# Kernel tuning notes

Hardware: AMD Instinct MI355X
Metric: run time of the kernel (lower is better)

## Reference

```python
import jax, jax.numpy as jnp
import numpy as np

_COLORS = np.array([
    [255, 255, 255], [219, 178, 187], [210, 144, 98], [230, 79, 56], [207, 62, 108],
    [130, 44, 28], [91, 31, 58], [209, 215, 63], [194, 202, 119], [224, 148, 36],
    [105, 147, 29], [131, 104, 50], [115, 233, 72], [189, 211, 189], [109, 215, 133],
    [72, 131, 77], [69, 81, 65], [77, 212, 193], [101, 159, 190], [120, 142, 215],
    [121, 102, 215], [111, 42, 240], [75, 42, 185], [57, 41, 119], [42, 46, 71],
    [216, 129, 199], [214, 67, 205], [147, 107, 128], [136, 48, 133], [0, 0, 0],
], dtype=np.float32) / 255.0  # [30, 3]

KH, KW = 5, 5
STRIDE = 1
EPS = 1e-8
NORM = 25.0 * 768.0


def _extract_patches(x, kh, kw, s):
    # x: [B, C, H, W] -> patches [B, C, h, w, kh, kw] (valid padding, stride s)
    B, C, H, W = x.shape
    h = (H - kh) // s + 1
    w = (W - kw) // s + 1
    cols = [x[:, :, i:i + s * h:s, j:j + s * w:s] for i in range(kh) for j in range(kw)]
    return jnp.stack(cols, axis=-1).reshape(B, C, h, w, kh, kw)


def setup_inputs() -> dict:
    key = jax.random.key(0)
    input_tensor = jax.random.uniform(key, (8, 3, 224, 224), dtype=jnp.float32)
    # learned parameter: 30 RGB prototype colors tiled over the kernel window
    weight = jnp.asarray(np.tile(_COLORS[:, :, None, None], (1, 1, KH, KW)))  # [30,3,5,5]
    return {"input_tensor": input_tensor, "weight": weight}


def reference(input_tensor, weight):
    kh, kw = weight.shape[2], weight.shape[3]
    p = _extract_patches(input_tensor, kh, kw, STRIDE)  # [B,3,h,w,kh,kw]
    # windows: [B,1,h,w,kh,kw]; weights: [1,30,1,1,kh,kw] -> broadcast [B,30,h,w,kh,kw]
    R1 = p[:, 0][:, None] * 255.0
    G1 = p[:, 1][:, None] * 255.0
    B1 = p[:, 2][:, None] * 255.0
    w255 = weight * 255.0
    R2 = w255[:, 0][None, :, None, None]
    G2 = w255[:, 1][None, :, None, None]
    B2 = w255[:, 2][None, :, None, None]
    rmean = (R1 + R2) * 0.5
    dR = R1 - R2
    dG = G1 - G2
    dB = B1 - B2
    d = jnp.sqrt((2.0 + rmean / 256.0) * dR * dR
                 + 4.0 * dG * dG
                 + (2.0 + (255.0 - rmean) / 256.0) * dB * dB
                 + EPS)
    return d.sum(axis=(-2, -1)) / NORM  # [B, 30, h, w]
```

## Files before the change

### kernel.cpp

```cpp
#include <hip/hip_runtime.h>
#include <hip/hip_fp16.h>
#include <math.h>

#define HDIM 224
#define WDIM 224
#define HW (HDIM * WDIM)
#define OH 220
#define OW 220
#define NCOL 30
#define TY 8
#define DROWS 12
#define NC4 56
#define NCELL (DROWS * NC4)
#define WSTR 116
#define NTILE 28
#define SCALE (16.0f / (25.0f * 768.0f))

__device__ __forceinline__ float4 ld4(const float* p) {
    return *reinterpret_cast<const float4*>(p);
}
__device__ __forceinline__ uint32_t h2u(__half2 h) { return __builtin_bit_cast(uint32_t, h); }
__device__ __forceinline__ __half2 u2h(uint32_t u) { return __builtin_bit_cast(__half2, u); }

__global__ __launch_bounds__(256, 8) void rgb_conv2d_kernel(
    const float* __restrict__ in,
    const float* __restrict__ wt,
    float* __restrict__ out)
{
    __shared__ uint32_t Dd[DROWS * WSTR];

    const int tid = threadIdx.x;
    const int by  = blockIdx.x;
    const int bc  = blockIdx.y;
    const int y0  = (by < NTILE - 1) ? by * TY : (OH - TY);
    const int b   = bc / NCOL;
    const int c   = bc - b * NCOL;

    const float* inb = in + (size_t)b * 3 * HW;
    const float R2f = wt[c * 75 +  0] * 255.0f;
    const float G2f = wt[c * 75 + 25] * 255.0f;
    const float B2f = wt[c * 75 + 50] * 255.0f;

    const __half2 hS    = __float2half2_rn(15.9375f);
    const __half2 hSG   = __float2half2_rn(31.875f);
    const __half2 hC512 = __float2half2_rn(255.0f / 512.0f);
    const __half2 hKR   = __float2half2_rn(fmaf(R2f, 1.0f / 512.0f, 2.0f));
    const __half2 hCC   = __float2half2_rn(4.0f + 255.0f / 256.0f);
    const __half2 hmR   = __float2half2_rn(-R2f * (1.0f / 16.0f));
    const __half2 hmG   = __float2half2_rn(-G2f * (1.0f / 8.0f));
    const __half2 hmB   = __float2half2_rn(-B2f * (1.0f / 16.0f));

    auto dist2 = [&](__half2 r, __half2 g, __half2 bb) -> __half2 {
        __half2 dR = __hfma2(r, hS, hmR);
        __half2 cR = __hfma2(r, hC512, hKR);
        __half2 cB = __hsub2(hCC, cR);
        __half2 dG = __hfma2(g, hSG, hmG);
        __half2 dB = __hfma2(bb, hS, hmB);
        __half2 t  = __hmul2(__hmul2(cR, dR), dR);
        t = __hfma2(dG, dG, t);
        t = __hfma2(__hmul2(cB, dB), dB, t);
        return h2sqrt(t);
    };

    #pragma unroll
    for (int p = 0; p < 3; ++p) {
        int idx = tid + p * 256;
        if (p < 2 || idx < NCELL) {
            int row  = idx / NC4;
            int col4 = idx - row * NC4;
            const float* src = inb + (y0 + row) * WDIM + 4 * col4;
            float4 Pr = ld4(src);
            float4 Pg = ld4(src + HW);
            float4 Pb = ld4(src + 2 * HW);
            __half2 rA = __floats2half2_rn(Pr.x, Pr.y), rB = __floats2half2_rn(Pr.z, Pr.w);
            __half2 gA = __floats2half2_rn(Pg.x, Pg.y), gB = __floats2half2_rn(Pg.z, Pg.w);
            __half2 bA = __floats2half2_rn(Pb.x, Pb.y), bB = __floats2half2_rn(Pb.z, Pb.w);
            __half2 dA = dist2(rA, gA, bA);
            __half2 dB = dist2(rB, gB, bB);
            *reinterpret_cast<uint2*>(&Dd[row * WSTR + 2 * col4]) =
                make_uint2(h2u(dA), h2u(dB));
        }
    }
    __syncthreads();

    if (tid < 220) {
        const int tx = tid % 55;
        const int g2 = tid / 55;
        const uint32_t* dp = &Dd[(2 * g2) * WSTR + 2 * tx];

        __half2 HA[6], HB[6];
        #pragma unroll
        for (int r = 0; r < 6; ++r) {
            uint2 v0 = *reinterpret_cast<const uint2*>(dp + r * WSTR);
            uint2 v1 = *reinterpret_cast<const uint2*>(dp + r * WSTR + 2);
            uint32_t a = v0.x, bw = v0.y, cw = v1.x, e = v1.y;
            __half2 t1 = u2h(__builtin_amdgcn_alignbit(bw, a, 16));
            __half2 t2 = u2h(__builtin_amdgcn_alignbit(cw, bw, 16));
            __half2 t3 = u2h(__builtin_amdgcn_alignbit(e, cw, 16));
            __half2 s  = __hadd2(__hadd2(u2h(bw), t2), u2h(cw));
            HA[r] = __hadd2(s, __hadd2(u2h(a), t1));
            HB[r] = __hadd2(s, __hadd2(t3, u2h(e)));
        }

        __half2 VA0 = __hadd2(__hadd2(__hadd2(HA[0], HA[1]), __hadd2(HA[2], HA[3])), HA[4]);
        __half2 VB0 = __hadd2(__hadd2(__hadd2(HB[0], HB[1]), __hadd2(HB[2], HB[3])), HB[4]);
        __half2 VA1 = __hadd2(__hsub2(VA0, HA[0]), HA[5]);
        __half2 VB1 = __hadd2(__hsub2(VB0, HB[0]), HB[5]);

        float* ob = out + ((size_t)bc * OH + (y0 + 2 * g2)) * OW + 4 * tx;
        *reinterpret_cast<float4*>(ob) =
            make_float4(__low2float(VA0) * SCALE, __high2float(VA0) * SCALE,
                        __low2float(VB0) * SCALE, __high2float(VB0) * SCALE);
        *reinterpret_cast<float4*>(ob + OW) =
            make_float4(__low2float(VA1) * SCALE, __high2float(VA1) * SCALE,
                        __low2float(VB1) * SCALE, __high2float(VB1) * SCALE);
    }
}

extern "C" void kernel_launch(void* const* d_in, const int* in_sizes, int n_in,
                              void* d_out, int out_size, void* d_ws, size_t ws_size,
                              hipStream_t stream) {
    const float* in = (const float*)d_in[0];
    const float* wt = (const float*)d_in[1];
    float* out = (float*)d_out;

    const int B = in_sizes[0] / (3 * HW);
    dim3 grid(NTILE, B * NCOL);
    rgb_conv2d_kernel<<<grid, dim3(256), 0, stream>>>(in, wt, out);
}
```

Before: 21.65 us.

## Process 55-row panels per block with persistent loop and nontemporal stores

Each block now covers a 55-row panel in five 11-row iterations instead of a single 8-row tile. That cuts the halo recompute overhead from 12/8 to 15/11 rows and lowers the block count. The grid is 1D with batch as the fastest index, so blocks that share a color are spread over different images. Outputs go out through nontemporal stores. The cost is an extra barrier per iteration, less parallelism, and uneven 3- or 2-row output work per thread group.

```diff
diff --git a/kernel.cpp b/kernel.cpp
--- a/kernel.cpp
+++ b/kernel.cpp
@@ -1,6 +1,5 @@
 #include <hip/hip_runtime.h>
 #include <hip/hip_fp16.h>
-#include <math.h>
 
 #define HDIM 224
 #define WDIM 224
@@ -8,13 +7,16 @@
 #define OH 220
 #define OW 220
 #define NCOL 30
-#define TY 8
-#define DROWS 12
+#define TY 11
+#define DROWS 15
 #define NC4 56
 #define NCELL (DROWS * NC4)
 #define WSTR 116
-#define NTILE 28
+#define NIT 5
+#define PANEL 55
 #define SCALE (16.0f / (25.0f * 768.0f))
+
+typedef float f4 __attribute__((ext_vector_type(4)));
 
 __device__ __forceinline__ float4 ld4(const float* p) {
     return *reinterpret_cast<const float4*>(p);
@@ -22,21 +24,31 @@
 __device__ __forceinline__ uint32_t h2u(__half2 h) { return __builtin_bit_cast(uint32_t, h); }
 __device__ __forceinline__ __half2 u2h(uint32_t u) { return __builtin_bit_cast(__half2, u); }
 
-__global__ __launch_bounds__(256, 8) void rgb_conv2d_kernel(
+__device__ __forceinline__ void st_nt(float* p, __half2 a, __half2 b) {
+    f4 v = { __low2float(a) * SCALE, __high2float(a) * SCALE,
+             __low2float(b) * SCALE, __high2float(b) * SCALE };
+    __builtin_nontemporal_store(v, reinterpret_cast<f4*>(p));
+}
+
+__global__ __launch_bounds__(256) void rgb_conv2d_kernel(
     const float* __restrict__ in,
     const float* __restrict__ wt,
-    float* __restrict__ out)
+    float* __restrict__ out,
+    int B)
 {
     __shared__ uint32_t Dd[DROWS * WSTR];
 
     const int tid = threadIdx.x;
-    const int by  = blockIdx.x;
-    const int bc  = blockIdx.y;
-    const int y0  = (by < NTILE - 1) ? by * TY : (OH - TY);
-    const int b   = bc / NCOL;
-    const int c   = bc - b * NCOL;
+    const int L   = blockIdx.x;
+    const int b   = L % B;
+    const int j   = L / B;
+    const int c   = j >> 2;
+    const int by  = j & 3;
+    const int y0  = by * PANEL;
 
     const float* inb = in + (size_t)b * 3 * HW;
+    const int bc = b * NCOL + c;
+
     const float R2f = wt[c * 75 +  0] * 255.0f;
     const float G2f = wt[c * 75 + 25] * 255.0f;
     const float B2f = wt[c * 75 + 50] * 255.0f;
@@ -62,58 +74,67 @@
         return h2sqrt(t);
     };
 
-    #pragma unroll
-    for (int p = 0; p < 3; ++p) {
-        int idx = tid + p * 256;
-        if (p < 2 || idx < NCELL) {
-            int row  = idx / NC4;
-            int col4 = idx - row * NC4;
-            const float* src = inb + (y0 + row) * WDIM + 4 * col4;
-            float4 Pr = ld4(src);
-            float4 Pg = ld4(src + HW);
-            float4 Pb = ld4(src + 2 * HW);
-            __half2 rA = __floats2half2_rn(Pr.x, Pr.y), rB = __floats2half2_rn(Pr.z, Pr.w);
-            __half2 gA = __floats2half2_rn(Pg.x, Pg.y), gB = __floats2half2_rn(Pg.z, Pg.w);
-            __half2 bA = __floats2half2_rn(Pb.x, Pb.y), bB = __floats2half2_rn(Pb.z, Pb.w);
-            __half2 dA = dist2(rA, gA, bA);
-            __half2 dB = dist2(rB, gB, bB);
-            *reinterpret_cast<uint2*>(&Dd[row * WSTR + 2 * col4]) =
-                make_uint2(h2u(dA), h2u(dB));
+    const int tx = tid % 55;
+    const int g  = tid / 55;
+    const int rg = 3 * g;
+    const int nr = (g < 3) ? 3 : 2;
+
+    for (int it = 0; it < NIT; ++it) {
+        const int yb = y0 + it * TY;
+
+        #pragma unroll
+        for (int p = 0; p < 4; ++p) {
+            int idx = tid + p * 256;
+            if (p < 3 || idx < NCELL) {
+                int row  = idx / NC4;
+                int col4 = idx - row * NC4;
+                const float* src = inb + (yb + row) * WDIM + 4 * col4;
+                float4 Pr = ld4(src);
+                float4 Pg = ld4(src + HW);
+                float4 Pb = ld4(src + 2 * HW);
+                __half2 rA = __floats2half2_rn(Pr.x, Pr.y), rB = __floats2half2_rn(Pr.z, Pr.w);
+                __half2 gA = __floats2half2_rn(Pg.x, Pg.y), gB = __floats2half2_rn(Pg.z, Pg.w);
+                __half2 bA = __floats2half2_rn(Pb.x, Pb.y), bB = __floats2half2_rn(Pb.z, Pb.w);
+                __half2 dA = dist2(rA, gA, bA);
+                __half2 dB = dist2(rB, gB, bB);
+                *reinterpret_cast<uint2*>(&Dd[row * WSTR + 2 * col4]) =
+                    make_uint2(h2u(dA), h2u(dB));
+            }
         }
-    }
-    __syncthreads();
+        __syncthreads();
 
-    if (tid < 220) {
-        const int tx = tid % 55;
-        const int g2 = tid / 55;
-        const uint32_t* dp = &Dd[(2 * g2) * WSTR + 2 * tx];
+        if (tid < 220) {
+            const uint32_t* dp = &Dd[rg * WSTR + 2 * tx];
+            __half2 HA[7], HB[7];
+            #pragma unroll
+            for (int r = 0; r < 7; ++r) {
+                if (r < nr + 4) {
+                    uint2 v0 = *reinterpret_cast<const uint2*>(dp + r * WSTR);
+                    uint2 v1 = *reinterpret_cast<const uint2*>(dp + r * WSTR + 2);
+                    uint32_t a = v0.x, bw = v0.y, cw = v1.x, e = v1.y;
+                    __half2 t1 = u2h(__builtin_amdgcn_alignbit(bw, a, 16));
+                    __half2 t2 = u2h(__builtin_amdgcn_alignbit(cw, bw, 16));
+                    __half2 t3 = u2h(__builtin_amdgcn_alignbit(e, cw, 16));
+                    __half2 s  = __hadd2(__hadd2(u2h(bw), t2), u2h(cw));
+                    HA[r] = __hadd2(s, __hadd2(u2h(a), t1));
+                    HB[r] = __hadd2(s, __hadd2(t3, u2h(e)));
+                }
+            }
 
-        __half2 HA[6], HB[6];
-        #pragma unroll
-        for (int r = 0; r < 6; ++r) {
-            uint2 v0 = *reinterpret_cast<const uint2*>(dp + r * WSTR);
-            uint2 v1 = *reinterpret_cast<const uint2*>(dp + r * WSTR + 2);
-            uint32_t a = v0.x, bw = v0.y, cw = v1.x, e = v1.y;
-            __half2 t1 = u2h(__builtin_amdgcn_alignbit(bw, a, 16));
-            __half2 t2 = u2h(__builtin_amdgcn_alignbit(cw, bw, 16));
-            __half2 t3 = u2h(__builtin_amdgcn_alignbit(e, cw, 16));
-            __half2 s  = __hadd2(__hadd2(u2h(bw), t2), u2h(cw));
-            HA[r] = __hadd2(s, __hadd2(u2h(a), t1));
-            HB[r] = __hadd2(s, __hadd2(t3, u2h(e)));
+            float* ob = out + ((size_t)bc * OH + (yb + rg)) * OW + 4 * tx;
+            __half2 VA = __hadd2(__hadd2(__hadd2(HA[0], HA[1]), __hadd2(HA[2], HA[3])), HA[4]);
+            __half2 VB = __hadd2(__hadd2(__hadd2(HB[0], HB[1]), __hadd2(HB[2], HB[3])), HB[4]);
+            st_nt(ob, VA, VB);
+            VA = __hadd2(__hsub2(VA, HA[0]), HA[5]);
+            VB = __hadd2(__hsub2(VB, HB[0]), HB[5]);
+            st_nt(ob + OW, VA, VB);
+            if (nr == 3) {
+                VA = __hadd2(__hsub2(VA, HA[1]), HA[6]);
+                VB = __hadd2(__hsub2(VB, HB[1]), HB[6]);
+                st_nt(ob + 2 * OW, VA, VB);
+            }
         }
-
-        __half2 VA0 = __hadd2(__hadd2(__hadd2(HA[0], HA[1]), __hadd2(HA[2], HA[3])), HA[4]);
-        __half2 VB0 = __hadd2(__hadd2(__hadd2(HB[0], HB[1]), __hadd2(HB[2], HB[3])), HB[4]);
-        __half2 VA1 = __hadd2(__hsub2(VA0, HA[0]), HA[5]);
-        __half2 VB1 = __hadd2(__hsub2(VB0, HB[0]), HB[5]);
-
-        float* ob = out + ((size_t)bc * OH + (y0 + 2 * g2)) * OW + 4 * tx;
-        *reinterpret_cast<float4*>(ob) =
-            make_float4(__low2float(VA0) * SCALE, __high2float(VA0) * SCALE,
-                        __low2float(VB0) * SCALE, __high2float(VB0) * SCALE);
-        *reinterpret_cast<float4*>(ob + OW) =
-            make_float4(__low2float(VA1) * SCALE, __high2float(VA1) * SCALE,
-                        __low2float(VB1) * SCALE, __high2float(VB1) * SCALE);
+        __syncthreads();
     }
 }
 
@@ -125,6 +146,6 @@
     float* out = (float*)d_out;
 
     const int B = in_sizes[0] / (3 * HW);
-    dim3 grid(NTILE, B * NCOL);
-    rgb_conv2d_kernel<<<grid, dim3(256), 0, stream>>>(in, wt, out);
+    const int nblocks = B * NCOL * 4;
+    rgb_conv2d_kernel<<<dim3(nblocks), dim3(256), 0, stream>>>(in, wt, out, B);
 }
```

New measurement: 21.13 us. 1.02x faster.

## Replace shared-memory tiles with per-wave row strips using shuffles and rolling sums

Applied to the files above, without the earlier changes.

Each wavefront now handles an 11-row strip of one output channel and walks 15 input rows. The horizontal neighbours come from warp shuffles instead of LDS, and the vertical 5-row window is kept in registers as a rolling window. This drops the shared memory, the __syncthreads and the 12-row halo recompute for every 8 output rows, so redundant distance work falls from 12/8 to 15/11. In exchange each wave runs a serial 15-iteration dependent loop, 9 of 64 lanes sit idle, and the batch index is hardcoded as L&7, which assumes B=8.

```diff
diff --git a/kernel.cpp b/kernel.cpp
--- a/kernel.cpp
+++ b/kernel.cpp
@@ -1,6 +1,5 @@
 #include <hip/hip_runtime.h>
 #include <hip/hip_fp16.h>
-#include <math.h>
 
 #define HDIM 224
 #define WDIM 224
@@ -8,12 +7,9 @@
 #define OH 220
 #define OW 220
 #define NCOL 30
-#define TY 8
-#define DROWS 12
-#define NC4 56
-#define NCELL (DROWS * NC4)
-#define WSTR 116
-#define NTILE 28
+#define SROWS 11
+#define NSTRIP 20
+#define LROWS 15
 #define SCALE (16.0f / (25.0f * 768.0f))
 
 __device__ __forceinline__ float4 ld4(const float* p) {
@@ -22,21 +18,28 @@
 __device__ __forceinline__ uint32_t h2u(__half2 h) { return __builtin_bit_cast(uint32_t, h); }
 __device__ __forceinline__ __half2 u2h(uint32_t u) { return __builtin_bit_cast(__half2, u); }
 
-__global__ __launch_bounds__(256, 8) void rgb_conv2d_kernel(
+__global__ __launch_bounds__(256) void rgb_conv2d_kernel(
     const float* __restrict__ in,
     const float* __restrict__ wt,
-    float* __restrict__ out)
+    float* __restrict__ out,
+    int B)
 {
-    __shared__ uint32_t Dd[DROWS * WSTR];
+    const int L    = blockIdx.x;
+    const int b    = L & 7;
+    const int j    = L >> 3;
+    const int wid  = threadIdx.x >> 6;
+    const int lane = threadIdx.x & 63;
+    const int idx  = j * 4 + wid;
+    const int c    = idx / NSTRIP;
+    const int s    = idx - c * NSTRIP;
+    const int y0   = s * SROWS;
 
-    const int tid = threadIdx.x;
-    const int by  = blockIdx.x;
-    const int bc  = blockIdx.y;
-    const int y0  = (by < NTILE - 1) ? by * TY : (OH - TY);
-    const int b   = bc / NCOL;
-    const int c   = bc - b * NCOL;
+    const int  lc = min(lane, 55);
+    const bool st = lane < 55;
 
-    const float* inb = in + (size_t)b * 3 * HW;
+    const float* base = in + (size_t)b * 3 * HW + (size_t)y0 * WDIM + 4 * lc;
+    float* ob = out + ((size_t)(b * NCOL + c) * OH + y0) * OW + 4 * lc;
+
     const float R2f = wt[c * 75 +  0] * 255.0f;
     const float G2f = wt[c * 75 + 25] * 255.0f;
     const float B2f = wt[c * 75 + 50] * 255.0f;
@@ -62,58 +65,42 @@
         return h2sqrt(t);
     };
 
-    #pragma unroll
-    for (int p = 0; p < 3; ++p) {
-        int idx = tid + p * 256;
-        if (p < 2 || idx < NCELL) {
-            int row  = idx / NC4;
-            int col4 = idx - row * NC4;
-            const float* src = inb + (y0 + row) * WDIM + 4 * col4;
-            float4 Pr = ld4(src);
-            float4 Pg = ld4(src + HW);
-            float4 Pb = ld4(src + 2 * HW);
-            __half2 rA = __floats2half2_rn(Pr.x, Pr.y), rB = __floats2half2_rn(Pr.z, Pr.w);
-            __half2 gA = __floats2half2_rn(Pg.x, Pg.y), gB = __floats2half2_rn(Pg.z, Pg.w);
-            __half2 bA = __floats2half2_rn(Pb.x, Pb.y), bB = __floats2half2_rn(Pb.z, Pb.w);
-            __half2 dA = dist2(rA, gA, bA);
-            __half2 dB = dist2(rB, gB, bB);
-            *reinterpret_cast<uint2*>(&Dd[row * WSTR + 2 * col4]) =
-                make_uint2(h2u(dA), h2u(dB));
+    __half2 HA0, HA1, HA2, HA3, HA4;
+    __half2 HB0, HB1, HB2, HB3, HB4;
+
+    for (int r = 0; r < LROWS; ++r) {
+        const float* rp = base + r * WDIM;
+        float4 Pr = ld4(rp);
+        float4 Pg = ld4(rp + HW);
+        float4 Pb = ld4(rp + 2 * HW);
+        __half2 rA = __floats2half2_rn(Pr.x, Pr.y), rB = __floats2half2_rn(Pr.z, Pr.w);
+        __half2 gA = __floats2half2_rn(Pg.x, Pg.y), gB = __floats2half2_rn(Pg.z, Pg.w);
+        __half2 bA = __floats2half2_rn(Pb.x, Pb.y), bB = __floats2half2_rn(Pb.z, Pb.w);
+        __half2 dA = dist2(rA, gA, bA);
+        __half2 dB = dist2(rB, gB, bB);
+
+        uint32_t a  = h2u(dA);
+        uint32_t bw = h2u(dB);
+        uint32_t cw = (uint32_t)__shfl_down((int)a, 1, 64);
+        uint32_t e  = (uint32_t)__shfl_down((int)bw, 1, 64);
+
+        __half2 t1 = u2h(__builtin_amdgcn_alignbit(bw, a, 16));
+        __half2 t2 = u2h(__builtin_amdgcn_alignbit(cw, bw, 16));
+        __half2 t3 = u2h(__builtin_amdgcn_alignbit(e, cw, 16));
+        __half2 sm = __hadd2(__hadd2(u2h(bw), t2), u2h(cw));
+        __half2 nHA = __hadd2(sm, __hadd2(u2h(a), t1));
+        __half2 nHB = __hadd2(sm, __hadd2(t3, u2h(e)));
+
+        HA0 = HA1; HA1 = HA2; HA2 = HA3; HA3 = HA4; HA4 = nHA;
+        HB0 = HB1; HB1 = HB2; HB2 = HB3; HB3 = HB4; HB4 = nHB;
+
+        if (r >= 4 && st) {
+            __half2 VA = __hadd2(__hadd2(__hadd2(HA0, HA1), __hadd2(HA2, HA3)), HA4);
+            __half2 VB = __hadd2(__hadd2(__hadd2(HB0, HB1), __hadd2(HB2, HB3)), HB4);
+            *reinterpret_cast<float4*>(ob + (size_t)(r - 4) * OW) =
+                make_float4(__low2float(VA) * SCALE, __high2float(VA) * SCALE,
+                            __low2float(VB) * SCALE, __high2float(VB) * SCALE);
         }
-    }
-    __syncthreads();
-
-    if (tid < 220) {
-        const int tx = tid % 55;
-        const int g2 = tid / 55;
-        const uint32_t* dp = &Dd[(2 * g2) * WSTR + 2 * tx];
-
-        __half2 HA[6], HB[6];
-        #pragma unroll
-        for (int r = 0; r < 6; ++r) {
-            uint2 v0 = *reinterpret_cast<const uint2*>(dp + r * WSTR);
-            uint2 v1 = *reinterpret_cast<const uint2*>(dp + r * WSTR + 2);
-            uint32_t a = v0.x, bw = v0.y, cw = v1.x, e = v1.y;
-            __half2 t1 = u2h(__builtin_amdgcn_alignbit(bw, a, 16));
-            __half2 t2 = u2h(__builtin_amdgcn_alignbit(cw, bw, 16));
-            __half2 t3 = u2h(__builtin_amdgcn_alignbit(e, cw, 16));
-            __half2 s  = __hadd2(__hadd2(u2h(bw), t2), u2h(cw));
-            HA[r] = __hadd2(s, __hadd2(u2h(a), t1));
-            HB[r] = __hadd2(s, __hadd2(t3, u2h(e)));
-        }
-
-        __half2 VA0 = __hadd2(__hadd2(__hadd2(HA[0], HA[1]), __hadd2(HA[2], HA[3])), HA[4]);
-        __half2 VB0 = __hadd2(__hadd2(__hadd2(HB[0], HB[1]), __hadd2(HB[2], HB[3])), HB[4]);
-        __half2 VA1 = __hadd2(__hsub2(VA0, HA[0]), HA[5]);
-        __half2 VB1 = __hadd2(__hsub2(VB0, HB[0]), HB[5]);
-
-        float* ob = out + ((size_t)bc * OH + (y0 + 2 * g2)) * OW + 4 * tx;
-        *reinterpret_cast<float4*>(ob) =
-            make_float4(__low2float(VA0) * SCALE, __high2float(VA0) * SCALE,
-                        __low2float(VB0) * SCALE, __high2float(VB0) * SCALE);
-        *reinterpret_cast<float4*>(ob + OW) =
-            make_float4(__low2float(VA1) * SCALE, __high2float(VA1) * SCALE,
-                        __low2float(VB1) * SCALE, __high2float(VB1) * SCALE);
     }
 }
 
@@ -125,6 +112,6 @@
     float* out = (float*)d_out;
 
     const int B = in_sizes[0] / (3 * HW);
-    dim3 grid(NTILE, B * NCOL);
-    rgb_conv2d_kernel<<<grid, dim3(256), 0, stream>>>(in, wt, out);
+    const int nblocks = B * NCOL * NSTRIP / 4;
+    rgb_conv2d_kernel<<<dim3(nblocks), dim3(256), 0, stream>>>(in, wt, out, B);
 }
```

After: 20.20 us. 6.7% less time.
